# Kernel tuning notes

Measured on AMD Instinct MI355X. Metric: run time of the kernel, lower is better.

The kernel has to match this reference:

```python
import jax, jax.numpy as jnp
import numpy as np

LOG_ZERO = -40.0
LOG_EPS = 1e-10

@jax.custom_vjp
def grad_scale(x):
    return x

def _gs_fwd(x):
    return x, None

def _gs_bwd(_, g):
    return (g * 0.01,)

grad_scale.defvjp(_gs_fwd, _gs_bwd)

def to_log_space(x):
    sign_x = jnp.sign(x)
    sign_x = jnp.where(sign_x == 0, jnp.ones_like(sign_x), sign_x)
    abs_x = jnp.abs(x)
    log_x = jnp.where(abs_x > LOG_EPS, jnp.log(jnp.maximum(abs_x, LOG_EPS)), LOG_ZERO)
    return log_x, sign_x

def from_log_space(log_x, sign_x):
    mask = log_x > LOG_ZERO + 1.0
    res = sign_x * jnp.exp(jnp.minimum(grad_scale(log_x), 20.0))
    return jnp.where(mask, res, jnp.zeros_like(res))

def signed_log_add(log_a, sign_a, log_b, sign_b):
    a_is_zero = log_a <= LOG_ZERO + 1.0
    b_is_zero = log_b <= LOG_ZERO + 1.0
    max_log = jnp.maximum(log_a, log_b)
    min_log = jnp.minimum(log_a, log_b)
    diff = min_log - max_log
    a_is_max = log_a >= log_b
    sign_max = jnp.where(a_is_max, sign_a, sign_b)
    sign_min = jnp.where(a_is_max, sign_b, sign_a)
    same_sign = sign_max * sign_min > 0
    exp_diff = jnp.exp(diff)
    log_same = max_log + jnp.log1p(exp_diff)
    log_opp = max_log + jnp.log1p(-jnp.minimum(exp_diff, 0.9999))
    log_result = jnp.where(same_sign, log_same, log_opp)
    sign_result = sign_max
    log_result = jnp.where(a_is_zero, log_b, log_result)
    sign_result = jnp.where(a_is_zero, sign_b, sign_result)
    log_result = jnp.where(b_is_zero & ~a_is_zero, log_a, log_result)
    sign_result = jnp.where(b_is_zero & ~a_is_zero, sign_a, sign_result)
    return log_result, sign_result

def soft_bound_log(log_h):
    return -jax.nn.softplus(-log_h)


def setup_inputs() -> dict:
    key = jax.random.key(0)
    T, B, D = 512, 16, 1024
    k = jax.random.split(key, 4)
    xav = float(np.sqrt(6.0 / (D + D)))  # xavier_uniform bound base
    return {
        'x': jax.random.normal(k[0], (T, B, D), jnp.float32),
        'W_x': jax.random.uniform(k[1], (D, D), jnp.float32, -0.5 * xav, 0.5 * xav),
        'W_alpha': jax.random.uniform(k[2], (D, D), jnp.float32, -0.1 * xav, 0.1 * xav),
        'W_delta': jax.random.uniform(k[3], (D, D), jnp.float32, -0.1 * xav, 0.1 * xav),
        'b': jnp.zeros(D, jnp.float32),
        'b_alpha': jnp.zeros(D, jnp.float32),
        'b_delta': jnp.full((D,), -2.0, jnp.float32),
        'log_r_h': jnp.full((D,), -2.0, jnp.float32),
        'sign_r_h': jnp.ones(D, jnp.float32),
    }


def reference(x, W_x, W_alpha, W_delta, b, b_alpha, b_delta, log_r_h, sign_r_h):
    T, B, D = x.shape
    # Precompute all input projections (the compute-heavy GEMMs) in one shot.
    alpha_raw = jnp.einsum('tbd,ed->tbe', x, W_alpha) + b_alpha        # [T,B,D]
    alpha = 1.0 + jax.nn.softplus(alpha_raw)
    lin = jnp.einsum('tbd,ed->tbe', x, W_x) + b                        # [T,B,D]
    log_input, sign_input = to_log_space(lin)
    delta_raw = jnp.einsum('tbd,ed->tbe', x, W_delta) + b_delta        # [T,B,D]
    log_delta = jax.nn.log_sigmoid(delta_raw)
    log_1m_delta = jax.nn.log_sigmoid(-delta_raw)

    log_h0 = jnp.full((B, D), LOG_ZERO, x.dtype)
    sign_h0 = jnp.ones((B, D), x.dtype)

    def step(carry, inp):
        log_hp, sign_hp = carry
        a_t, log_in, sign_in, log_d, log_1md = inp
        log_rh = log_r_h + log_hp
        sign_rh = sign_r_h * sign_hp
        log_v, sign_v = signed_log_add(log_rh, sign_rh, log_in, sign_in)
        log_cand = soft_bound_log(a_t * log_v)
        log_h_new, sign_h_new = signed_log_add(log_1md + log_hp, sign_hp,
                                               log_d + log_cand, sign_v)
        h_lin = from_log_space(log_h_new, sign_h_new)
        return (log_h_new, sign_h_new), (log_h_new, sign_h_new, h_lin)

    _, (log_hs, sign_hs, h_linear) = jax.lax.scan(
        step, (log_h0, sign_h0), (alpha, log_input, sign_input, log_delta, log_1m_delta))
    log_h = jnp.concatenate([log_h0[None], log_hs], axis=0)    # [T+1,B,D]
    sign_h = jnp.concatenate([sign_h0[None], sign_hs], axis=0) # [T+1,B,D]
    return log_h, sign_h, h_linear
```

## Files before the change

kernel.cpp:

```cpp
#include <hip/hip_runtime.h>
#include <math.h>

#define BD 16384
#define TT 512
#define KDIM 1024
#define NDIM 1024
#define GEMM_M 8192
#define PANEL_Q 320
#define LOGE2F 0.69314718246459960938f

__device__ __forceinline__ float np_expf(float x)   { return expf(x); }
__device__ __forceinline__ float np_logf(float x)   { return logf(x); }
__device__ __forceinline__ float np_log1pf(float x) { return log1pf(x); }

__device__ __forceinline__ float np_softplus(float v) {
    const float e  = np_expf(-fabsf(v));
    const float l1 = np_log1pf(e);
    const float r  = __fadd_rn(fmaxf(v, 0.0f), l1);
    return (v == 0.0f) ? LOGE2F : r;
}

__device__ __forceinline__ void np_sla(float la, float sa, float lb, float sb,
                                       float& lo, float& so) {
    bool az = la <= -39.0f;
    bool bz = lb <= -39.0f;
    float mx = fmaxf(la, lb);
    float mn = fminf(la, lb);
    float diff = __fsub_rn(mn, mx);
    bool amax = la >= lb;
    float smax = amax ? sa : sb;
    float smin = amax ? sb : sa;
    bool same = __fmul_rn(smax, smin) > 0.0f;
    float ed = np_expf(diff);
    float arg = same ? ed : -fminf(ed, 0.9999f);
    float l = __fadd_rn(mx, np_log1pf(arg));
    float s = smax;
    l = az ? lb : l;  s = az ? sb : s;
    bool bo = bz && !az;
    l = bo ? la : l;  s = bo ? sa : s;
    lo = l; so = s;
}

__global__ __launch_bounds__(256, 4) void gemm_blas(
    const float* __restrict__ x,
    const float* __restrict__ Wa, const float* __restrict__ Wx, const float* __restrict__ Wd,
    const float* __restrict__ ba, const float* __restrict__ bx, const float* __restrict__ bd,
    float* __restrict__ out_a, float* __restrict__ out_x, float* __restrict__ out_d)
{
    const int z = blockIdx.z;
    const float* W    = (z == 0) ? Wa : (z == 1) ? Wx : Wd;
    const float* bias = (z == 0) ? ba : (z == 1) ? bx : bd;
    float* out        = (z == 0) ? out_a : (z == 1) ? out_x : out_d;

    const int m0 = blockIdx.x * 128;
    const int n0 = blockIdx.y * 64;

    __shared__ float As[16][132];
    __shared__ float Bs[16][68];

    const int tid = threadIdx.x;
    const int lr = tid >> 2;
    const int lc = tid & 3;
    const int ty = tid >> 4;
    const int tx = tid & 15;

    const float* Ap = x + (size_t)(m0 + lr) * KDIM + lc * 4;
    const float* Bp = W + (size_t)(n0 + lr) * KDIM + lc * 4;

    float4 aR0 = *(const float4*)(Ap);
    float4 aR1 = *(const float4*)(Ap + (size_t)64 * KDIM);
    float4 bR0 = *(const float4*)(Bp);

    float tot[8][4];
    float acc[8][4];
    #pragma unroll
    for (int i = 0; i < 8; ++i)
        #pragma unroll
        for (int j = 0; j < 4; ++j) { tot[i][j] = 0.0f; acc[i][j] = 0.0f; }

    for (int kt = 0; kt < KDIM; kt += 16) {
        if (kt == PANEL_Q || kt == 2 * PANEL_Q || kt == 3 * PANEL_Q) {
            #pragma unroll
            for (int i = 0; i < 8; ++i)
                #pragma unroll
                for (int j = 0; j < 4; ++j) {
                    tot[i][j] = __fadd_rn(tot[i][j], acc[i][j]);
                    acc[i][j] = 0.0f;
                }
        }
        __syncthreads();
        {
            const float* a0 = (const float*)&aR0;
            const float* a1 = (const float*)&aR1;
            const float* b0 = (const float*)&bR0;
            #pragma unroll
            for (int c = 0; c < 4; ++c) {
                As[lc * 4 + c][lr]      = a0[c];
                As[lc * 4 + c][lr + 64] = a1[c];
                Bs[lc * 4 + c][lr]      = b0[c];
            }
        }
        __syncthreads();
        if (kt + 16 < KDIM) {
            aR0 = *(const float4*)(Ap + kt + 16);
            aR1 = *(const float4*)(Ap + (size_t)64 * KDIM + kt + 16);
            bR0 = *(const float4*)(Bp + kt + 16);
        }
        #pragma unroll
        for (int kk = 0; kk < 16; ++kk) {
            const float4 a0 = *(const float4*)&As[kk][ty * 4];
            const float4 a1 = *(const float4*)&As[kk][64 + ty * 4];
            const float4 b0 = *(const float4*)&Bs[kk][tx * 4];
            const float av[8] = {a0.x, a0.y, a0.z, a0.w, a1.x, a1.y, a1.z, a1.w};
            const float bv[4] = {b0.x, b0.y, b0.z, b0.w};
            #pragma unroll
            for (int i = 0; i < 8; ++i)
                #pragma unroll
                for (int j = 0; j < 4; ++j)
                    acc[i][j] = __fmaf_rn(av[i], bv[j], acc[i][j]);
        }
    }
    #pragma unroll
    for (int i = 0; i < 8; ++i)
        #pragma unroll
        for (int j = 0; j < 4; ++j)
            tot[i][j] = __fadd_rn(tot[i][j], acc[i][j]);

    float bj[4];
    #pragma unroll
    for (int j = 0; j < 4; ++j) bj[j] = bias[n0 + tx * 4 + j];

    #pragma unroll
    for (int h = 0; h < 2; ++h) {
        #pragma unroll
        for (int i = 0; i < 4; ++i) {
            const int mi = h * 4 + i;
            float* op = out + (size_t)(m0 + h * 64 + ty * 4 + i) * NDIM + n0 + tx * 4;
            float4 v;
            v.x = __fadd_rn(tot[mi][0], bj[0]);
            v.y = __fadd_rn(tot[mi][1], bj[1]);
            v.z = __fadd_rn(tot[mi][2], bj[2]);
            v.w = __fadd_rn(tot[mi][3], bj[3]);
            *(float4*)op = v;
        }
    }
}

__device__ __forceinline__ void gl_lds(const float* g, float* l) {
    __builtin_amdgcn_global_load_lds(
        (const __attribute__((address_space(1))) void*)g,
        (__attribute__((address_space(3))) void*)l, 4, 0, 0);
}

#define WAITVM(N) do {                                                   \
    asm volatile("s_waitcnt vmcnt(" #N ")" ::: "memory");                \
    __builtin_amdgcn_sched_barrier(0); } while (0)

__global__ __launch_bounds__(192, 1) void scan_kernel(
    float* __restrict__ log_h, float* __restrict__ sign_h, float* __restrict__ h_lin,
    const float* __restrict__ log_r_h, const float* __restrict__ sign_r_h)
{
    __shared__ float Xr[4][5][4][64];
    __shared__ float Or[4][2][4][64];
    __shared__ float Rr[4][12][64];

    const int wv = threadIdx.x >> 6;
    const int ln = threadIdx.x & 63;
    const int idx = blockIdx.x * 64 + ln;

#define ISSUE_LOADS(GG, SL) do {                                         \
    const int _b = (GG) * 4;                                             \
    _Pragma("unroll")                                                    \
    for (int u = 0; u < 4; ++u) {                                        \
        gl_lds(h_lin  + (size_t)(_b + u) * BD + idx,     &Rr[SL][u * 3 + 0][0]); \
        gl_lds(log_h  + (size_t)(_b + u + 1) * BD + idx, &Rr[SL][u * 3 + 1][0]); \
        gl_lds(sign_h + (size_t)(_b + u + 1) * BD + idx, &Rr[SL][u * 3 + 2][0]); \
    } } while (0)

#define XFORM_TO(GG) do {                                                \
    const int _s = (GG) & 3;                                             \
    _Pragma("unroll")                                                    \
    for (int u = 0; u < 4; ++u) {                                        \
        const float araw = Rr[_s][u * 3 + 0][ln];                        \
        const float lin  = Rr[_s][u * 3 + 1][ln];                        \
        const float dr   = Rr[_s][u * 3 + 2][ln];                        \
        Xr[_s][0][u][ln] = __fadd_rn(1.0f, np_softplus(araw));           \
        const float ax = fabsf(lin);                                     \
        Xr[_s][1][u][ln] = (ax > 1e-10f) ? np_logf(fmaxf(ax, 1e-10f))    \
                                         : -40.0f;                       \
        Xr[_s][2][u][ln] = (lin < 0.0f) ? -1.0f : 1.0f;                  \
        const float e  = np_expf(-fabsf(dr));                            \
        const float l1 = np_log1pf(e);                                   \
        const float big = -__fadd_rn(fabsf(dr), l1);                     \
        const float sml = -l1;                                           \
        const float ld0 = (dr > 0.0f) ? sml : big;                       \
        const float lm0 = (dr > 0.0f) ? big : sml;                       \
        Xr[_s][3][u][ln] = (dr == 0.0f) ? -LOGE2F : ld0;                 \
        Xr[_s][4][u][ln] = (dr == 0.0f) ? -LOGE2F : lm0;                 \
    } } while (0)

#define WRITE_GROUP(GG) do {                                             \
    const int _s = (GG) & 3;                                             \
    _Pragma("unroll")                                                    \
    for (int u = 0; u < 4; ++u) {                                        \
        const int t = (GG) * 4 + u;                                      \
        const float lhn = Or[_s][0][u][ln];                              \
        const float shn = Or[_s][1][u][ln];                              \
        const float res = __fmul_rn(shn, np_expf(fminf(lhn, 20.0f)));    \
        const float h = (lhn > -39.0f) ? res : 0.0f;                     \
        log_h[(size_t)(t + 1) * BD + idx] = lhn;                         \
        sign_h[(size_t)(t + 1) * BD + idx] = shn;                        \
        h_lin[(size_t)t * BD + idx] = h;                                 \
    } } while (0)

    float lrh = 0.0f, srh = 0.0f;
    if (wv == 1) {
        const int d = idx & 1023;
        lrh = log_r_h[d];
        srh = sign_r_h[d];
    } else if (wv == 0) {
        ISSUE_LOADS(0, 0);
        ISSUE_LOADS(1, 1);
        WAITVM(0);
        XFORM_TO(0);
        XFORM_TO(1);
        ISSUE_LOADS(2, 2);
    } else {
        log_h[idx] = -40.0f;
        sign_h[idx] = 1.0f;
    }
    __syncthreads();

    float lhp = -40.0f, shp = 1.0f;

    for (int g = 0; g < 128; ++g) {
        if (wv == 0) {
            const int gl = (g + 3 < 128) ? g + 3 : 127;
            ISSUE_LOADS(gl, (g + 3) & 3);
            WAITVM(12);
            if (g + 2 < 128) XFORM_TO(g + 2);
        } else if (wv == 1) {
            const int s = g & 3;
            float xa[4], xli[4], xsi[4], xld[4], xlm[4];
            #pragma unroll
            for (int u = 0; u < 4; ++u) {
                xa[u]  = Xr[s][0][u][ln];
                xli[u] = Xr[s][1][u][ln];
                xsi[u] = Xr[s][2][u][ln];
                xld[u] = Xr[s][3][u][ln];
                xlm[u] = Xr[s][4][u][ln];
            }
            #pragma unroll
            for (int u = 0; u < 4; ++u) {
                const float log_rh  = __fadd_rn(lrh, lhp);
                const float sign_rh = __fmul_rn(srh, shp);
                float lv, sv;
                np_sla(log_rh, sign_rh, xli[u], xsi[u], lv, sv);
                const float tt = __fmul_rn(xa[u], lv);
                const float log_cand = -np_softplus(-tt);
                float lhn, shn;
                np_sla(__fadd_rn(xlm[u], lhp), shp,
                       __fadd_rn(xld[u], log_cand), sv, lhn, shn);
                Or[s][0][u][ln] = lhn;
                Or[s][1][u][ln] = shn;
                lhp = lhn; shp = shn;
            }
        } else {
            if (g > 0) WRITE_GROUP(g - 1);
        }
        __syncthreads();
    }
    if (wv == 2) WRITE_GROUP(127);

#undef ISSUE_LOADS
#undef XFORM_TO
#undef WRITE_GROUP
}

extern "C" void kernel_launch(void* const* d_in, const int* in_sizes, int n_in,
                              void* d_out, int out_size, void* d_ws, size_t ws_size,
                              hipStream_t stream) {
    const float* x        = (const float*)d_in[0];
    const float* W_x      = (const float*)d_in[1];
    const float* W_alpha  = (const float*)d_in[2];
    const float* W_delta  = (const float*)d_in[3];
    const float* b        = (const float*)d_in[4];
    const float* b_alpha  = (const float*)d_in[5];
    const float* b_delta  = (const float*)d_in[6];
    const float* log_r_h  = (const float*)d_in[7];
    const float* sign_r_h = (const float*)d_in[8];

    float* out    = (float*)d_out;
    float* log_h  = out;
    float* sign_h = out + (size_t)513 * BD;
    float* h_lin  = out + (size_t)2 * 513 * BD;

    dim3 ggrid(GEMM_M / 128, NDIM / 64, 3);
    gemm_blas<<<ggrid, dim3(256), 0, stream>>>(
        x, W_alpha, W_x, W_delta, b_alpha, b, b_delta,
        h_lin, log_h + BD, sign_h + BD);

    scan_kernel<<<dim3(BD / 64), dim3(192), 0, stream>>>(
        log_h, sign_h, h_lin, log_r_h, sign_r_h);
}
```

Baseline: 1.126 ms.

## Double-buffer GEMM shared tiles with a K-tile of 32 and one barrier per step

The projection GEMM now keeps two shared-memory buffers for the A and B tiles and doubles the K-tile from 16 to 32. Global loads for the next tile are issued before the FMA loop on the current tile, and only one __syncthreads runs per iteration instead of two. This aims to hide global-load latency behind compute and halve barrier overhead. In exchange, LDS per block roughly quadruples to about 51KB and the prefetch registers double, which can lower the resident blocks below the requested launch bound of four.

```diff
diff --git a/kernel.cpp b/kernel.cpp
--- a/kernel.cpp
+++ b/kernel.cpp
@@ -55,21 +55,23 @@
     const int m0 = blockIdx.x * 128;
     const int n0 = blockIdx.y * 64;
 
-    __shared__ float As[16][132];
-    __shared__ float Bs[16][68];
+    __shared__ float As[2][32][132];
+    __shared__ float Bs[2][32][68];
 
     const int tid = threadIdx.x;
-    const int lr = tid >> 2;
-    const int lc = tid & 3;
+    const int lc = tid & 7;
+    const int lr = tid >> 3;
     const int ty = tid >> 4;
     const int tx = tid & 15;
 
     const float* Ap = x + (size_t)(m0 + lr) * KDIM + lc * 4;
     const float* Bp = W + (size_t)(n0 + lr) * KDIM + lc * 4;
 
-    float4 aR0 = *(const float4*)(Ap);
-    float4 aR1 = *(const float4*)(Ap + (size_t)64 * KDIM);
-    float4 bR0 = *(const float4*)(Bp);
+    float4 a4[4], b4[2];
+    #pragma unroll
+    for (int r = 0; r < 4; ++r) a4[r] = *(const float4*)(Ap + (size_t)(r * 32) * KDIM);
+    #pragma unroll
+    for (int r = 0; r < 2; ++r) b4[r] = *(const float4*)(Bp + (size_t)(r * 32) * KDIM);
 
     float tot[8][4];
     float acc[8][4];
@@ -78,7 +80,32 @@
         #pragma unroll
         for (int j = 0; j < 4; ++j) { tot[i][j] = 0.0f; acc[i][j] = 0.0f; }
 
-    for (int kt = 0; kt < KDIM; kt += 16) {
+    {
+        #pragma unroll
+        for (int c = 0; c < 4; ++c) {
+            const float* pa0 = (const float*)&a4[0];
+            #pragma unroll
+            for (int r = 0; r < 4; ++r)
+                As[0][lc * 4 + c][lr + r * 32] = ((const float*)&a4[r])[c];
+            #pragma unroll
+            for (int r = 0; r < 2; ++r)
+                Bs[0][lc * 4 + c][lr + r * 32] = ((const float*)&b4[r])[c];
+            (void)pa0;
+        }
+    }
+    __syncthreads();
+
+    int cur = 0;
+    for (int kt = 0; kt < KDIM; kt += 32) {
+        const bool haveNext = (kt + 32 < KDIM);
+        if (haveNext) {
+            #pragma unroll
+            for (int r = 0; r < 4; ++r)
+                a4[r] = *(const float4*)(Ap + (size_t)(r * 32) * KDIM + kt + 32);
+            #pragma unroll
+            for (int r = 0; r < 2; ++r)
+                b4[r] = *(const float4*)(Bp + (size_t)(r * 32) * KDIM + kt + 32);
+        }
         if (kt == PANEL_Q || kt == 2 * PANEL_Q || kt == 3 * PANEL_Q) {
             #pragma unroll
             for (int i = 0; i < 8; ++i)
@@ -88,36 +115,32 @@
                     acc[i][j] = 0.0f;
                 }
         }
-        __syncthreads();
-        {
-            const float* a0 = (const float*)&aR0;
-            const float* a1 = (const float*)&aR1;
-            const float* b0 = (const float*)&bR0;
-            #pragma unroll
-            for (int c = 0; c < 4; ++c) {
-                As[lc * 4 + c][lr]      = a0[c];
-                As[lc * 4 + c][lr + 64] = a1[c];
-                Bs[lc * 4 + c][lr]      = b0[c];
-            }
-        }
-        __syncthreads();
-        if (kt + 16 < KDIM) {
-            aR0 = *(const float4*)(Ap + kt + 16);
-            aR1 = *(const float4*)(Ap + (size_t)64 * KDIM + kt + 16);
-            bR0 = *(const float4*)(Bp + kt + 16);
-        }
-        #pragma unroll
-        for (int kk = 0; kk < 16; ++kk) {
-            const float4 a0 = *(const float4*)&As[kk][ty * 4];
-            const float4 a1 = *(const float4*)&As[kk][64 + ty * 4];
-            const float4 b0 = *(const float4*)&Bs[kk][tx * 4];
-            const float av[8] = {a0.x, a0.y, a0.z, a0.w, a1.x, a1.y, a1.z, a1.w};
-            const float bv[4] = {b0.x, b0.y, b0.z, b0.w};
+        #pragma unroll
+        for (int kk = 0; kk < 32; ++kk) {
+            const float4 A0 = *(const float4*)&As[cur][kk][ty * 4];
+            const float4 A1 = *(const float4*)&As[cur][kk][64 + ty * 4];
+            const float4 B0 = *(const float4*)&Bs[cur][kk][tx * 4];
+            const float av[8] = {A0.x, A0.y, A0.z, A0.w, A1.x, A1.y, A1.z, A1.w};
+            const float bv[4] = {B0.x, B0.y, B0.z, B0.w};
             #pragma unroll
             for (int i = 0; i < 8; ++i)
                 #pragma unroll
                 for (int j = 0; j < 4; ++j)
                     acc[i][j] = __fmaf_rn(av[i], bv[j], acc[i][j]);
+        }
+        if (haveNext) {
+            const int nxt = cur ^ 1;
+            #pragma unroll
+            for (int c = 0; c < 4; ++c) {
+                #pragma unroll
+                for (int r = 0; r < 4; ++r)
+                    As[nxt][lc * 4 + c][lr + r * 32] = ((const float*)&a4[r])[c];
+                #pragma unroll
+                for (int r = 0; r < 2; ++r)
+                    Bs[nxt][lc * 4 + c][lr + r * 32] = ((const float*)&b4[r])[c];
+            }
+            __syncthreads();
+            cur = nxt;
         }
     }
     #pragma unroll
```

Measured after the change: 1.119 ms. No clear change (-0.6%).
